# Kernel optimization log

Hardware: AMD Instinct MI355X
Metric: run time of the kernel (lower is better)

## Reference

```python
import jax, jax.numpy as jnp
import numpy as np

V, C, DFF, NH, NL, KS, OUT = 256, 192, 768, 2, 6, 3, 192
B, T, W = 64, 512, 4
DH = C // NH
PAD = KS // 2
DN = ('NCH', 'OIH', 'NCH')


def _rel_to_abs(x):
    # [b,h,l,2l-1] -> [b,h,l,l]  (VITS _relative_position_to_absolute_position)
    b, h, l, _ = x.shape
    x = jnp.pad(x, ((0, 0), (0, 0), (0, 0), (0, 1)))
    x = x.reshape(b, h, l * 2 * l)
    x = jnp.pad(x, ((0, 0), (0, 0), (0, l - 1)))
    x = x.reshape(b, h, l + 1, 2 * l - 1)
    return x[:, :, :l, l - 1:]


def _abs_to_rel(x):
    # [b,h,l,l] -> [b,h,l,2l-1]  (VITS _absolute_position_to_relative_position)
    b, h, l, _ = x.shape
    x = jnp.pad(x, ((0, 0), (0, 0), (0, 0), (0, l - 1)))
    x = x.reshape(b, h, l * (2 * l - 1))
    x = jnp.pad(x, ((0, 0), (0, 0), (l, 0)))
    x = x.reshape(b, h, l, 2 * l)
    return x[:, :, :, 1:]


def _get_rel_emb(emb, length):
    # emb: [2W+1, DH] -> [2*length-1, DH]
    pad_len = max(length - (W + 1), 0)
    start = max(W + 1 - length, 0)
    padded = jnp.pad(emb, ((pad_len, pad_len), (0, 0)))
    return padded[start:start + 2 * length - 1]


def _ln(x, g, b):
    mu = jnp.mean(x, -1, keepdims=True)
    var = jnp.mean(jnp.square(x - mu), -1, keepdims=True)
    return (x - mu) * jax.lax.rsqrt(var + 1e-5) * g + b


def setup_inputs():
    key = jax.random.key(0)
    ks = jax.random.split(key, 12)
    n = lambda k, s, std: jax.random.normal(k, s, jnp.float32) * std
    return dict(
        tokens=jax.random.randint(ks[0], (B, T), 0, V),
        x_lengths=jnp.full((B,), T, dtype=jnp.int32),
        emb_w=n(ks[1], (V, C), C ** -0.5),
        wqkv=n(ks[2], (NL, 3, C, C), 0.02),
        bqkv=jnp.zeros((NL, 3, C), jnp.float32),
        wo=n(ks[3], (NL, C, C), 0.02),
        bo=jnp.zeros((NL, C), jnp.float32),
        rel_k=n(ks[4], (NL, 2 * W + 1, DH), DH ** -0.5),
        rel_v=n(ks[5], (NL, 2 * W + 1, DH), DH ** -0.5),
        ln1_g=jnp.ones((NL, C), jnp.float32),
        ln1_b=jnp.zeros((NL, C), jnp.float32),
        ln2_g=jnp.ones((NL, C), jnp.float32),
        ln2_b=jnp.zeros((NL, C), jnp.float32),
        ffn_w1=n(ks[6], (NL, DFF, C, KS), 0.02),
        ffn_b1=jnp.zeros((NL, DFF), jnp.float32),
        ffn_w2=n(ks[7], (NL, C, DFF, KS), 0.02),
        ffn_b2=jnp.zeros((NL, C), jnp.float32),
        proj_w=n(ks[8], (2 * OUT, C), 0.02),
        proj_b=jnp.zeros((2 * OUT,), jnp.float32),
    )


def reference(tokens, x_lengths, emb_w, wqkv, bqkv, wo, bo, rel_k, rel_v,
              ln1_g, ln1_b, ln2_g, ln2_b, ffn_w1, ffn_b1, ffn_w2, ffn_b2,
              proj_w, proj_b):
    x = emb_w[tokens] * (C ** 0.5)                       # [B,T,C]
    mask = (jnp.arange(T)[None, :] < x_lengths[:, None]).astype(x.dtype)  # [B,T]
    bias = jnp.where((mask[:, None, :, None] * mask[:, None, None, :]) > 0.0, 0.0, -1e4)
    x = x * mask[..., None]
    inv_sqrt_d = DH ** -0.5
    for l in range(NL):
        q = jnp.einsum('btc,oc->bto', x, wqkv[l, 0]) + bqkv[l, 0]
        k = jnp.einsum('btc,oc->bto', x, wqkv[l, 1]) + bqkv[l, 1]
        v = jnp.einsum('btc,oc->bto', x, wqkv[l, 2]) + bqkv[l, 2]
        q = q.reshape(B, T, NH, DH).transpose(0, 2, 1, 3)  # [B,H,T,D]
        k = k.reshape(B, T, NH, DH).transpose(0, 2, 1, 3)
        v = v.reshape(B, T, NH, DH).transpose(0, 2, 1, 3)
        scores = jnp.einsum('bhtd,bhsd->bhts', q, k) * inv_sqrt_d
        rk = _get_rel_emb(rel_k[l], T)                     # [2T-1, D]
        rel_logits = jnp.einsum('bhtd,md->bhtm', q * inv_sqrt_d, rk)
        scores = scores + _rel_to_abs(rel_logits)
        p = jax.nn.softmax(scores + bias, axis=-1)
        o = jnp.einsum('bhts,bhsd->bhtd', p, v)
        o = o + jnp.einsum('bhtm,md->bhtd', _abs_to_rel(p), _get_rel_emb(rel_v[l], T))
        o = o.transpose(0, 2, 1, 3).reshape(B, T, C)
        y = jnp.einsum('btc,oc->bto', o, wo[l]) + bo[l]
        x = _ln(x + y, ln1_g[l], ln1_b[l])
        h = jax.lax.conv_general_dilated((x * mask[..., None]).transpose(0, 2, 1),
                                         ffn_w1[l], (1,), [(PAD, PAD)],
                                         dimension_numbers=DN) + ffn_b1[l][None, :, None]
        h = jax.nn.relu(h) * mask[:, None, :]
        h = jax.lax.conv_general_dilated(h, ffn_w2[l], (1,), [(PAD, PAD)],
                                         dimension_numbers=DN) + ffn_b2[l][None, :, None]
        y = h.transpose(0, 2, 1) * mask[..., None]
        x = _ln(x + y, ln2_g[l], ln2_b[l])
    x = x * mask[..., None]
    stats = (jnp.einsum('btc,oc->bto', x, proj_w) + proj_b) * mask[..., None]
    m, logs = jnp.split(stats, 2, axis=-1)
    x_mask = mask[:, None, :]
    return x.transpose(0, 2, 1), m.transpose(0, 2, 1), logs.transpose(0, 2, 1), x_mask
```

## Files before the change

kernel.cpp:

```cpp
#include <hip/hip_runtime.h>
#include <hip/hip_bf16.h>

typedef __hip_bfloat16 bf16;
typedef __attribute__((ext_vector_type(8))) short short8;
typedef __attribute__((ext_vector_type(4))) float f32x4;

#define NB 64
#define NT 512
#define NC 192
#define NHEAD 2
#define NDH 96
#define NLAYER 6
#define NDFF 768
#define NW 4

constexpr int MROWS = NB * NT;
constexpr size_t MC = (size_t)MROWS * NC;
constexpr size_t MCB = MC * 4;
constexpr float QSC = 0.10206207261596575f * 1.4426950408889634f;

__device__ __forceinline__ float us2f(unsigned short x) { return __uint_as_float((unsigned)x << 16); }
__device__ __forceinline__ unsigned short f2b(float f) {
    bf16 h = __float2bfloat16(f);
    return *reinterpret_cast<unsigned short*>(&h);
}

__global__ __launch_bounds__(256) void cvt_plain(const float* __restrict__ s, bf16* __restrict__ d, int n) {
    int i = blockIdx.x * 256 + threadIdx.x;
    if (i < n) d[i] = __float2bfloat16(s[i]);
}
__global__ __launch_bounds__(256) void cvt_conv(const float* __restrict__ s, bf16* __restrict__ d,
                                                int L, int N, int C) {
    int i = blockIdx.x * 256 + threadIdx.x;
    if (i >= L * N * C * 3) return;
    int dk = i % 3;
    int rest = i / 3;
    int c = rest % C;
    int rest2 = rest / C;
    int n = rest2 % N;
    int l = rest2 / N;
    d[(((size_t)l * 3 + dk) * N + n) * C + c] = __float2bfloat16(s[i]);
}

__global__ __launch_bounds__(256) void embed_kernel(const int* __restrict__ tok,
                                                    const int* __restrict__ lens,
                                                    const float* __restrict__ emb,
                                                    float* __restrict__ x,
                                                    bf16* __restrict__ xb) {
    int idx = blockIdx.x * 256 + threadIdx.x;
    if (idx >= (int)MC) return;
    int c = idx % NC;
    int m = idx / NC;
    int t = m % NT, b = m / NT;
    float v = emb[tok[m] * NC + c] * 13.856406460551018f;
    if (t >= lens[b]) v = 0.f;
    x[idx] = v;
    xb[idx] = __float2bfloat16(v);
}

enum GMode { GM_QKV = 0, GM_CONV1 = 2, GM_PROJ = 4 };

template <int MODE, int NTOT, int KC, int TAPS>
__global__ __launch_bounds__(256) void gemm_mfma(const bf16* __restrict__ A,
                                                 const bf16* __restrict__ W,
                                                 const float* __restrict__ bias,
                                                 const int* __restrict__ lens,
                                                 float* __restrict__ of,
                                                 bf16* __restrict__ ob1,
                                                 bf16* __restrict__ ob2,
                                                 bf16* __restrict__ ob3) {
    constexpr int RA = (TAPS == 3) ? 130 : 128;
    constexpr int RB = TAPS * 64;
    __shared__ unsigned short As[RA * 40];
    __shared__ unsigned short Bs[RB * 40];
    const int tid = threadIdx.x;
    const int w = tid >> 6, lane = tid & 63;
    const int g = lane >> 4, li = lane & 15;
    const int n0 = blockIdx.x * 64;
    const int m0 = blockIdx.y * 128;
    const int b = m0 >> 9, t0 = m0 & 511;
    const int len = lens[b];
    const unsigned short* Au = (const unsigned short*)A;
    const unsigned short* Wu = (const unsigned short*)W;

    f32x4 acc[2][4];
#pragma unroll
    for (int a = 0; a < 2; a++)
#pragma unroll
        for (int s = 0; s < 4; s++) acc[a][s] = (f32x4){0.f, 0.f, 0.f, 0.f};

#pragma unroll 1
    for (int k0 = 0; k0 < KC; k0 += 32) {
        __syncthreads();
        for (int c = tid; c < RA * 2; c += 256) {
            int i = c >> 1, hf = (c & 1) * 16;
            int t = t0 + i - (TAPS == 3 ? 1 : 0);
            bool valid = (t >= 0) && (t < NT);
            if constexpr (MODE == GM_CONV1) valid = valid && (t < len);
            short8 v0{}, v1{};
            if (valid) {
                const unsigned short* src = Au + ((size_t)(b * NT + t) * KC + k0 + hf);
                v0 = *(const short8*)src;
                v1 = *(const short8*)(src + 8);
            }
            *(short8*)&As[i * 40 + hf] = v0;
            *(short8*)&As[i * 40 + hf + 8] = v1;
        }
        for (int c = tid; c < RB * 4; c += 256) {
            int rb = c >> 2, qq = (c & 3) * 8;
            int dk = rb >> 6, nl = rb & 63;
            *(short8*)&Bs[rb * 40 + qq] =
                *(const short8*)(Wu + ((size_t)(dk * NTOT + n0 + nl) * KC + k0 + qq));
        }
        __syncthreads();
#pragma unroll
        for (int dk = 0; dk < TAPS; dk++) {
            short8 af0 = *(const short8*)&As[(w * 32 + li + dk) * 40 + g * 8];
            short8 af1 = *(const short8*)&As[(w * 32 + 16 + li + dk) * 40 + g * 8];
#pragma unroll
            for (int sub = 0; sub < 4; sub++) {
                short8 bfr = *(const short8*)&Bs[(dk * 64 + sub * 16 + li) * 40 + g * 8];
                acc[0][sub] = __builtin_amdgcn_mfma_f32_16x16x32_bf16(af0, bfr, acc[0][sub], 0, 0, 0);
                acc[1][sub] = __builtin_amdgcn_mfma_f32_16x16x32_bf16(af1, bfr, acc[1][sub], 0, 0, 0);
            }
        }
    }

#pragma unroll
    for (int sub = 0; sub < 4; sub++) {
        int n = n0 + sub * 16 + li;
        float bv = bias[n];
#pragma unroll
        for (int a = 0; a < 2; a++) {
#pragma unroll
            for (int rr = 0; rr < 4; rr++) {
                int t = t0 + w * 32 + a * 16 + g * 4 + rr;
                size_t m = (size_t)(b * NT + t);
                float vv = acc[a][sub][rr] + bv;
                if constexpr (MODE == GM_QKV) {
                    int iw = n / NC;
                    int cc = n - iw * NC;
                    int hh = cc >= NDH ? 1 : 0;
                    int d = cc - hh * NDH;
                    int bh = b * NHEAD + hh;
                    if (iw == 0) ob1[((size_t)bh * NT + t) * NDH + d] = __float2bfloat16(vv * QSC);
                    else if (iw == 1) ob2[((size_t)bh * NT + t) * NDH + d] = __float2bfloat16(vv);
                    else ob3[((size_t)bh * NDH + d) * NT + t] = __float2bfloat16(vv);
                } else if constexpr (MODE == GM_CONV1) {
                    vv = vv > 0.f ? vv : 0.f;
                    if (t >= len) vv = 0.f;
                    ob1[m * NDFF + n] = __float2bfloat16(vv);
                } else {
                    if (t >= len) vv = 0.f;
                    int half = n >= 192 ? 1 : 0;
                    int cc = n - half * 192;
                    of[(size_t)(half + 1) * MC + ((size_t)b * NC + cc) * NT + t] = vv;
                }
            }
        }
    }
}

template <int KC, int TAPS, bool MASKY, int BM>
__global__ __launch_bounds__(512) void gemm_ln(const bf16* __restrict__ A,
                                               const bf16* __restrict__ W,
                                               const float* __restrict__ bias,
                                               const int* __restrict__ lens,
                                               const float* __restrict__ lng,
                                               const float* __restrict__ lnb,
                                               float* __restrict__ x,
                                               bf16* __restrict__ xb) {
    constexpr int RA = BM + ((TAPS == 3) ? 2 : 0);
    constexpr int RB = TAPS * 192;
    constexpr int NSTEP = KC / 32;
    constexpr int NBI = (RB * 4 + 511) / 512;
    constexpr int AR = BM / 32;
    __shared__ unsigned short As[RA * 40];
    __shared__ unsigned short Bs[RB * 40];
    __shared__ float rsm[BM][4];
    __shared__ float rsq[BM][4];
    const int tid = threadIdx.x;
    const int lane = tid & 63;
    const int g = lane >> 4, li = lane & 15;
    const int w = tid >> 6;
    const int wr = w & 1, wc = w >> 1;
    const int m0 = blockIdx.x * BM;
    const int b = m0 >> 9, t0 = m0 & 511;
    const int len = lens[b];
    const unsigned short* Au = (const unsigned short*)A;
    const unsigned short* Wu = (const unsigned short*)W;

    const int ai = tid >> 1, ahf = (tid & 1) * 16;
    const int at = t0 + ai - (TAPS == 3 ? 1 : 0);
    const bool aon = (tid < RA * 2);
    const bool avalid = aon && (at >= 0) && (at < NT);

    short8 ra0{}, ra1{};
    short8 rbv[NBI];
#pragma unroll
    for (int j = 0; j < NBI; j++) rbv[j] = short8{};

    f32x4 acc[AR][3];
#pragma unroll
    for (int ar = 0; ar < AR; ar++)
#pragma unroll
        for (int sub = 0; sub < 3; sub++) acc[ar][sub] = (f32x4){0.f, 0.f, 0.f, 0.f};

    if (avalid) {
        const unsigned short* src = Au + ((size_t)(b * NT + at) * KC + 0 + ahf);
        ra0 = *(const short8*)src;
        ra1 = *(const short8*)(src + 8);
    }
#pragma unroll
    for (int j = 0; j < NBI; j++) {
        int cb = tid + j * 512;
        if (cb < RB * 4) {
            int rbr = cb >> 2, qq = (cb & 3) * 8;
            rbv[j] = *(const short8*)(Wu + ((size_t)rbr * KC + 0 + qq));
        }
    }
    if (aon) {
        short8 z{};
        *(short8*)&As[ai * 40 + ahf] = avalid ? ra0 : z;
        *(short8*)&As[ai * 40 + ahf + 8] = avalid ? ra1 : z;
    }
#pragma unroll
    for (int j = 0; j < NBI; j++) {
        int cb = tid + j * 512;
        if (cb < RB * 4) {
            int rbr = cb >> 2, qq = (cb & 3) * 8;
            *(short8*)&Bs[rbr * 40 + qq] = rbv[j];
        }
    }

#pragma unroll 1
    for (int s = 0; s < NSTEP; s++) {
        __syncthreads();
        if (s + 1 < NSTEP) {
            int k0 = (s + 1) * 32;
            if (avalid) {
                const unsigned short* src = Au + ((size_t)(b * NT + at) * KC + k0 + ahf);
                ra0 = *(const short8*)src;
                ra1 = *(const short8*)(src + 8);
            }
#pragma unroll
            for (int j = 0; j < NBI; j++) {
                int cb = tid + j * 512;
                if (cb < RB * 4) {
                    int rbr = cb >> 2, qq = (cb & 3) * 8;
                    rbv[j] = *(const short8*)(Wu + ((size_t)rbr * KC + k0 + qq));
                }
            }
        }
#pragma unroll
        for (int dk = 0; dk < TAPS; dk++) {
            short8 af[AR];
#pragma unroll
            for (int ar = 0; ar < AR; ar++)
                af[ar] = *(const short8*)&As[(wr * (BM / 2) + ar * 16 + li + dk) * 40 + g * 8];
#pragma unroll
            for (int sub = 0; sub < 3; sub++) {
                short8 bfr = *(const short8*)&Bs[(dk * 192 + wc * 48 + sub * 16 + li) * 40 + g * 8];
#pragma unroll
                for (int ar = 0; ar < AR; ar++)
                    acc[ar][sub] = __builtin_amdgcn_mfma_f32_16x16x32_bf16(af[ar], bfr, acc[ar][sub], 0, 0, 0);
            }
        }
        __syncthreads();
        if (s + 1 < NSTEP) {
            if (aon) {
                short8 z{};
                *(short8*)&As[ai * 40 + ahf] = avalid ? ra0 : z;
                *(short8*)&As[ai * 40 + ahf + 8] = avalid ? ra1 : z;
            }
#pragma unroll
            for (int j = 0; j < NBI; j++) {
                int cb = tid + j * 512;
                if (cb < RB * 4) {
                    int rbr = cb >> 2, qq = (cb & 3) * 8;
                    *(short8*)&Bs[rbr * 40 + qq] = rbv[j];
                }
            }
        }
    }

    float biasv[3], gv[3], bbv[3];
#pragma unroll
    for (int sub = 0; sub < 3; sub++) {
        int n = wc * 48 + sub * 16 + li;
        biasv[sub] = bias[n];
        gv[sub] = lng[n];
        bbv[sub] = lnb[n];
    }
    float psm[AR][4], psq[AR][4];
#pragma unroll
    for (int ar = 0; ar < AR; ar++) {
#pragma unroll
        for (int rr = 0; rr < 4; rr++) {
            int r = wr * (BM / 2) + ar * 16 + 4 * g + rr;
            int t = t0 + r;
            size_t m = (size_t)(b * NT + t);
            float sm = 0.f, sq = 0.f;
#pragma unroll
            for (int sub = 0; sub < 3; sub++) {
                int n = wc * 48 + sub * 16 + li;
                float y = acc[ar][sub][rr] + biasv[sub];
                if (MASKY && t >= len) y = 0.f;
                float rres = y + x[m * NC + n];
                acc[ar][sub][rr] = rres;
                sm += rres;
                sq += rres * rres;
            }
            psm[ar][rr] = sm;
            psq[ar][rr] = sq;
        }
    }
#pragma unroll
    for (int off = 1; off < 16; off <<= 1) {
#pragma unroll
        for (int ar = 0; ar < AR; ar++)
#pragma unroll
            for (int rr = 0; rr < 4; rr++) {
                psm[ar][rr] += __shfl_xor(psm[ar][rr], off);
                psq[ar][rr] += __shfl_xor(psq[ar][rr], off);
            }
    }
    if (li == 0) {
#pragma unroll
        for (int ar = 0; ar < AR; ar++)
#pragma unroll
            for (int rr = 0; rr < 4; rr++) {
                int r = wr * (BM / 2) + ar * 16 + 4 * g + rr;
                rsm[r][wc] = psm[ar][rr];
                rsq[r][wc] = psq[ar][rr];
            }
    }
    __syncthreads();
#pragma unroll
    for (int ar = 0; ar < AR; ar++) {
#pragma unroll
        for (int rr = 0; rr < 4; rr++) {
            int r = wr * (BM / 2) + ar * 16 + 4 * g + rr;
            int t = t0 + r;
            size_t m = (size_t)(b * NT + t);
            float sm = rsm[r][0] + rsm[r][1] + rsm[r][2] + rsm[r][3];
            float sq = rsq[r][0] + rsq[r][1] + rsq[r][2] + rsq[r][3];
            float mu = sm * (1.f / NC);
            float var = fmaxf(sq * (1.f / NC) - mu * mu, 0.f);
            float rs = rsqrtf(var + 1e-5f);
#pragma unroll
            for (int sub = 0; sub < 3; sub++) {
                int n = wc * 48 + sub * 16 + li;
                float o = (acc[ar][sub][rr] - mu) * rs * gv[sub] + bbv[sub];
                x[m * NC + n] = o;
                xb[m * NC + n] = __float2bfloat16(o);
            }
        }
    }
}

__global__ __launch_bounds__(256, 4) void attn_mfma(const bf16* __restrict__ q,
                                                    const bf16* __restrict__ k,
                                                    const bf16* __restrict__ v,
                                                    const float* __restrict__ relk,
                                                    const float* __restrict__ relv,
                                                    const int* __restrict__ lens,
                                                    bf16* __restrict__ o) {
    __shared__ __align__(16) char pool[40448];
    unsigned short* Kt = (unsigned short*)pool;
    unsigned short* Vt = (unsigned short*)(pool + 13312);
    unsigned short* Pt = (unsigned short*)(pool + 27136);
    unsigned short* Pb = (unsigned short*)(pool + 36352);
    unsigned short* Qt = (unsigned short*)pool;
    unsigned short* Rk = (unsigned short*)(pool + 13312);

    const int bh = blockIdx.x, qt = blockIdx.y;
    const int b = bh >> 1, h = bh & 1;
    const int q0 = qt * 64;
    const int tid = threadIdx.x;
    const int w = tid >> 6, lane = tid & 63;
    const int g = lane >> 4, li = lane & 15;
    const int len = lens[b];
    const bool anymask = (len < NT);

    const unsigned short* qg = (const unsigned short*)q + (size_t)bh * NT * NDH;
    const unsigned short* kg = (const unsigned short*)k + (size_t)bh * NT * NDH;
    const unsigned short* vg = (const unsigned short*)v + (size_t)bh * NDH * NT;

    for (int c = tid; c < 64 * 12; c += 256) {
        int r = c / 12, seg = (c % 12) * 8;
        *(short8*)&Qt[r * 104 + seg] = *(const short8*)(qg + (size_t)(q0 + r) * NDH + seg);
    }
    for (int c = tid; c < 16 * 96; c += 256) {
        int dd = c / 96, d = c - (c / 96) * 96;
        Rk[dd * 104 + d] = (dd < 9) ? f2b(relk[dd * 96 + d]) : (unsigned short)0;
    }
    for (int c = tid; c < 4 * 16 * 32; c += 256) Pb[c] = 0;
    __syncthreads();

    f32x4 racc = (f32x4){0.f, 0.f, 0.f, 0.f};
    short8 qf[3];
#pragma unroll
    for (int kk = 0; kk < 3; kk++) {
        qf[kk] = *(const short8*)&Qt[(w * 16 + li) * 104 + kk * 32 + g * 8];
        short8 bfr = *(const short8*)&Rk[li * 104 + kk * 32 + g * 8];
        racc = __builtin_amdgcn_mfma_f32_16x16x32_bf16(qf[kk], bfr, racc, 0, 0, 0);
    }
    short8 rvf[6];
#pragma unroll
    for (int ds = 0; ds < 6; ds++) {
#pragma unroll
        for (int i = 0; i < 8; i++) {
            int j = g * 8 + i;
            int d = ds * 16 + li;
            unsigned short u = (j < 9) ? f2b(relv[j * 96 + d]) : (unsigned short)0;
            rvf[ds][i] = (short)u;
        }
    }
    __syncthreads();

    float m_run[4], l_run[4];
    f32x4 Oa[6];
#pragma unroll
    for (int rr = 0; rr < 4; rr++) { m_run[rr] = -1e30f; l_run[rr] = 0.f; }
#pragma unroll
    for (int ds = 0; ds < 6; ds++) Oa[ds] = (f32x4){0.f, 0.f, 0.f, 0.f};

    const int wrow0 = q0 + w * 16;

    for (int s0 = 0; s0 < NT; s0 += 64) {
        for (int c = tid; c < 64 * 12; c += 256) {
            int ss = c / 12, seg = (c % 12) * 8;
            *(short8*)&Kt[ss * 104 + seg] = *(const short8*)(kg + (size_t)(s0 + ss) * NDH + seg);
        }
        for (int c = tid; c < 96 * 8; c += 256) {
            int d = c >> 3, seg = (c & 7) * 8;
            *(short8*)&Vt[d * 72 + seg] = *(const short8*)(vg + (size_t)d * NT + s0 + seg);
        }
        __syncthreads();

        const bool band = (s0 <= wrow0 + 15 + NW) && (s0 + 63 >= wrow0 - NW);

        f32x4 acc[4];
#pragma unroll
        for (int sub = 0; sub < 4; sub++) acc[sub] = (f32x4){0.f, 0.f, 0.f, 0.f};
        __builtin_amdgcn_s_setprio(1);
#pragma unroll
        for (int kk = 0; kk < 3; kk++) {
#pragma unroll
            for (int sub = 0; sub < 4; sub++) {
                short8 bfr = *(const short8*)&Kt[(sub * 16 + li) * 104 + kk * 32 + g * 8];
                acc[sub] = __builtin_amdgcn_mfma_f32_16x16x32_bf16(qf[kk], bfr, acc[sub], 0, 0, 0);
            }
        }
        __builtin_amdgcn_s_setprio(0);

        if (band) {
#pragma unroll
            for (int sub = 0; sub < 4; sub++) {
#pragma unroll
                for (int rr = 0; rr < 4; rr++) {
                    int scol = s0 + sub * 16 + li;
                    int qrow = wrow0 + 4 * g + rr;
                    int dd = scol - qrow;
                    float rv = __shfl(racc[rr], g * 16 + dd + NW);
                    if (dd >= -NW && dd <= NW) acc[sub][rr] += rv;
                }
            }
        }
        float rmax[4];
#pragma unroll
        for (int rr = 0; rr < 4; rr++) rmax[rr] = -1e30f;
#pragma unroll
        for (int sub = 0; sub < 4; sub++) {
#pragma unroll
            for (int rr = 0; rr < 4; rr++) {
                if (anymask) {
                    int scol = s0 + sub * 16 + li;
                    int qrow = wrow0 + 4 * g + rr;
                    if (scol >= len || qrow >= len) acc[sub][rr] -= 14427.0f;
                }
                rmax[rr] = fmaxf(rmax[rr], acc[sub][rr]);
            }
        }
#pragma unroll
        for (int off = 1; off < 16; off <<= 1)
#pragma unroll
            for (int rr = 0; rr < 4; rr++) rmax[rr] = fmaxf(rmax[rr], __shfl_xor(rmax[rr], off));

        float growth = -3.0e38f;
#pragma unroll
        for (int rr = 0; rr < 4; rr++) growth = fmaxf(growth, rmax[rr] - m_run[rr]);
        if (__any(growth > 11.54f)) {
#pragma unroll
            for (int rr = 0; rr < 4; rr++) {
                float mn = fmaxf(m_run[rr], rmax[rr]);
                float scf = exp2f(m_run[rr] - mn);
                m_run[rr] = mn;
                l_run[rr] *= scf;
#pragma unroll
                for (int ds = 0; ds < 6; ds++) Oa[ds][rr] *= scf;
            }
        }
        float rsum[4] = {0.f, 0.f, 0.f, 0.f};
#pragma unroll
        for (int sub = 0; sub < 4; sub++)
#pragma unroll
            for (int rr = 0; rr < 4; rr++) {
                float p = exp2f(acc[sub][rr] - m_run[rr]);
                acc[sub][rr] = p;
                rsum[rr] += p;
            }
#pragma unroll
        for (int off = 1; off < 16; off <<= 1)
#pragma unroll
            for (int rr = 0; rr < 4; rr++) rsum[rr] += __shfl_xor(rsum[rr], off);
#pragma unroll
        for (int rr = 0; rr < 4; rr++) l_run[rr] += rsum[rr];

#pragma unroll
        for (int sub = 0; sub < 4; sub++)
#pragma unroll
            for (int rr = 0; rr < 4; rr++)
                Pt[w * 1152 + (4 * g + rr) * 72 + sub * 16 + li] = f2b(acc[sub][rr]);

        __builtin_amdgcn_s_setprio(1);
#pragma unroll
        for (int kk = 0; kk < 2; kk++) {
            short8 pa = *(const short8*)&Pt[w * 1152 + li * 72 + kk * 32 + g * 8];
#pragma unroll
            for (int ds = 0; ds < 6; ds++) {
                short8 bv = *(const short8*)&Vt[(ds * 16 + li) * 72 + kk * 32 + g * 8];
                Oa[ds] = __builtin_amdgcn_mfma_f32_16x16x32_bf16(pa, bv, Oa[ds], 0, 0, 0);
            }
        }
        __builtin_amdgcn_s_setprio(0);

        if (band) {
            for (int j = g; j < 9; j += 4) {
                int u = wrow0 + li + j - NW - s0;
                unsigned short pv_ = (u >= 0 && u < 64) ? Pt[w * 1152 + li * 72 + u] : (unsigned short)0;
                Pb[w * 512 + li * 32 + j] = pv_;
            }
            short8 pband = *(const short8*)&Pb[w * 512 + li * 32 + g * 8];
#pragma unroll
            for (int ds = 0; ds < 6; ds++)
                Oa[ds] = __builtin_amdgcn_mfma_f32_16x16x32_bf16(pband, rvf[ds], Oa[ds], 0, 0, 0);
        }
        __syncthreads();
    }

    float invl[4];
#pragma unroll
    for (int rr = 0; rr < 4; rr++) invl[rr] = 1.f / l_run[rr];
#pragma unroll
    for (int ds = 0; ds < 6; ds++)
#pragma unroll
        for (int rr = 0; rr < 4; rr++) {
            int qrow = wrow0 + 4 * g + rr;
            o[((size_t)(b * NT + qrow)) * NC + h * 96 + ds * 16 + li] =
                __float2bfloat16(Oa[ds][rr] * invl[rr]);
        }
}

__global__ __launch_bounds__(256) void xpose_kernel(const float* __restrict__ x,
                                                    const int* __restrict__ lens,
                                                    float* __restrict__ out) {
    int idx = blockIdx.x * 256 + threadIdx.x;
    if (idx >= (int)MC) return;
    int t = idx % NT;
    int bc = idx / NT;
    int c = bc % NC;
    int b = bc / NC;
    float v = (t < lens[b]) ? x[((size_t)b * NT + t) * NC + c] : 0.f;
    out[idx] = v;
}

__global__ __launch_bounds__(256) void mask_kernel(const int* __restrict__ lens, float* __restrict__ out) {
    int idx = blockIdx.x * 256 + threadIdx.x;
    if (idx >= NB * NT) return;
    int t = idx % NT;
    int b = idx / NT;
    out[idx] = (t < lens[b]) ? 1.f : 0.f;
}

extern "C" void kernel_launch(void* const* d_in, const int* in_sizes, int n_in,
                              void* d_out, int out_size, void* d_ws, size_t ws_size,
                              hipStream_t stream) {
    (void)in_sizes; (void)n_in; (void)out_size; (void)ws_size;
    const int* tok = (const int*)d_in[0];
    const int* lens = (const int*)d_in[1];
    const float* emb = (const float*)d_in[2];
    const float* wqkv = (const float*)d_in[3];
    const float* bqkv = (const float*)d_in[4];
    const float* wo = (const float*)d_in[5];
    const float* bo = (const float*)d_in[6];
    const float* relk = (const float*)d_in[7];
    const float* relv = (const float*)d_in[8];
    const float* ln1g = (const float*)d_in[9];
    const float* ln1b = (const float*)d_in[10];
    const float* ln2g = (const float*)d_in[11];
    const float* ln2b = (const float*)d_in[12];
    const float* fw1 = (const float*)d_in[13];
    const float* fb1 = (const float*)d_in[14];
    const float* fw2 = (const float*)d_in[15];
    const float* fb2 = (const float*)d_in[16];
    const float* pw = (const float*)d_in[17];
    const float* pb = (const float*)d_in[18];
    float* out = (float*)d_out;

    char* wsb = (char*)d_ws;
    float* xB = (float*)wsb;
    bf16* xb = (bf16*)(wsb + 2 * MCB);
    bf16* qb = (bf16*)(wsb + 2 * MCB + MCB / 2);
    bf16* kb = qb + MC;
    bf16* vb = kb + MC;
    bf16* ob = vb + MC;
    bf16* hB = qb;
    bf16* pwqkv = ob + MC;
    bf16* pwo = pwqkv + (size_t)NLAYER * 3 * NC * NC;
    bf16* pw1 = pwo + (size_t)NLAYER * NC * NC;
    bf16* pw2 = pw1 + (size_t)NLAYER * 3 * NDFF * NC;
    bf16* pproj = pw2 + (size_t)NLAYER * 3 * NC * NDFF;

    {
        int n1 = NLAYER * 3 * NC * NC;
        cvt_plain<<<(n1 + 255) / 256, 256, 0, stream>>>(wqkv, pwqkv, n1);
        int n2 = NLAYER * NC * NC;
        cvt_plain<<<(n2 + 255) / 256, 256, 0, stream>>>(wo, pwo, n2);
        int n3 = 2 * 192 * NC;
        cvt_plain<<<(n3 + 255) / 256, 256, 0, stream>>>(pw, pproj, n3);
        int n4 = NLAYER * NDFF * NC * 3;
        cvt_conv<<<(n4 + 255) / 256, 256, 0, stream>>>(fw1, pw1, NLAYER, NDFF, NC);
        int n5 = NLAYER * NC * NDFF * 3;
        cvt_conv<<<(n5 + 255) / 256, 256, 0, stream>>>(fw2, pw2, NLAYER, NC, NDFF);
    }

    embed_kernel<<<(int)((MC + 255) / 256), 256, 0, stream>>>(tok, lens, emb, xB, xb);

    for (int l = 0; l < NLAYER; l++) {
        gemm_mfma<GM_QKV, 576, 192, 1><<<dim3(9, 256), 256, 0, stream>>>(
            xb, pwqkv + (size_t)l * 3 * NC * NC, bqkv + (size_t)l * 3 * NC, lens,
            nullptr, qb, kb, vb);
        attn_mfma<<<dim3(NB * NHEAD, 8), 256, 0, stream>>>(
            qb, kb, vb, relk + (size_t)l * (2 * NW + 1) * NDH,
            relv + (size_t)l * (2 * NW + 1) * NDH, lens, ob);
        gemm_ln<192, 1, false, 64><<<512, 512, 0, stream>>>(
            ob, pwo + (size_t)l * NC * NC, bo + (size_t)l * NC, lens,
            ln1g + (size_t)l * NC, ln1b + (size_t)l * NC, xB, xb);
        gemm_mfma<GM_CONV1, 768, 192, 3><<<dim3(12, 256), 256, 0, stream>>>(
            xb, pw1 + (size_t)l * 3 * NDFF * NC, fb1 + (size_t)l * NDFF, lens,
            nullptr, hB, nullptr, nullptr);
        gemm_ln<768, 3, true, 64><<<512, 512, 0, stream>>>(
            hB, pw2 + (size_t)l * 3 * NC * NDFF, fb2 + (size_t)l * NC, lens,
            ln2g + (size_t)l * NC, ln2b + (size_t)l * NC, xB, xb);
    }

    gemm_mfma<GM_PROJ, 384, 192, 1><<<dim3(6, 256), 256, 0, stream>>>(
        xb, pproj, pb, lens, out, nullptr, nullptr, nullptr);
    xpose_kernel<<<(int)((MC + 255) / 256), 256, 0, stream>>>(xB, lens, out);
    mask_kernel<<<(NB * NT + 255) / 256, 256, 0, stream>>>(lens, out + 3 * MC);
}
```

Baseline: 1.507 ms.

## Pre-swizzle weights into MFMA fragment order and load B directly from global

Weight conversion kernels now write bf16 weights in a per-lane MFMA fragment layout, so each lane can fetch its B operand with a single 16-byte global load. Both GEMM kernels drop the shared-memory B tile and its staging loops, and gemm_ln double-buffers B fragments in registers across K steps. gemm_ln also gets a min-blocks hint of 4 in its launch bounds. This removes LDS traffic and LDS capacity for weights, at the cost of more registers and repeated global or L2 reads of the weights by every wave.

After: 1.448 ms. 1.04x faster.

```diff
diff --git a/kernel.cpp b/kernel.cpp
--- a/kernel.cpp
+++ b/kernel.cpp
@@ -25,21 +25,43 @@
     return *reinterpret_cast<unsigned short*>(&h);
 }
 
-__global__ __launch_bounds__(256) void cvt_plain(const float* __restrict__ s, bf16* __restrict__ d, int n) {
+__global__ __launch_bounds__(256) void cvt_frag_plain(const float* __restrict__ s, bf16* __restrict__ d,
+                                                      int L, int N, int K) {
     int i = blockIdx.x * 256 + threadIdx.x;
-    if (i < n) d[i] = __float2bfloat16(s[i]);
-}
-__global__ __launch_bounds__(256) void cvt_conv(const float* __restrict__ s, bf16* __restrict__ d,
-                                                int L, int N, int C) {
+    int total = L * (N / 16) * (K / 32) * 64;
+    if (i >= total) return;
+    int lane = i & 63;
+    int tile = i >> 6;
+    int nbk = K / 32;
+    int kb = tile % nbk;
+    int rest = tile / nbk;
+    int nb = rest % (N / 16);
+    int l = rest / (N / 16);
+    int li = lane & 15, g = lane >> 4;
+    const float* src = s + ((size_t)l * N + nb * 16 + li) * K + kb * 32 + g * 8;
+    bf16* dst = d + (size_t)i * 8;
+#pragma unroll
+    for (int u = 0; u < 8; u++) dst[u] = __float2bfloat16(src[u]);
+}
+__global__ __launch_bounds__(256) void cvt_frag_conv(const float* __restrict__ s, bf16* __restrict__ d,
+                                                     int L, int N, int C) {
     int i = blockIdx.x * 256 + threadIdx.x;
-    if (i >= L * N * C * 3) return;
-    int dk = i % 3;
-    int rest = i / 3;
-    int c = rest % C;
-    int rest2 = rest / C;
-    int n = rest2 % N;
-    int l = rest2 / N;
-    d[(((size_t)l * 3 + dk) * N + n) * C + c] = __float2bfloat16(s[i]);
+    int total = L * 3 * (N / 16) * (C / 32) * 64;
+    if (i >= total) return;
+    int lane = i & 63;
+    int tile = i >> 6;
+    int nbk = C / 32;
+    int kb = tile % nbk;
+    int rest = tile / nbk;
+    int nb = rest % (N / 16);
+    int rest2 = rest / (N / 16);
+    int dk = rest2 % 3;
+    int l = rest2 / 3;
+    int li = lane & 15, g = lane >> 4;
+    const float* src = s + (((size_t)l * N + nb * 16 + li) * C + kb * 32 + g * 8) * 3 + dk;
+    bf16* dst = d + (size_t)i * 8;
+#pragma unroll
+    for (int u = 0; u < 8; u++) dst[u] = __float2bfloat16(src[u * 3]);
 }
 
 __global__ __launch_bounds__(256) void embed_kernel(const int* __restrict__ tok,
@@ -70,9 +92,9 @@
                                                  bf16* __restrict__ ob2,
                                                  bf16* __restrict__ ob3) {
     constexpr int RA = (TAPS == 3) ? 130 : 128;
-    constexpr int RB = TAPS * 64;
+    constexpr int NBN = NTOT / 16;
+    constexpr int NBK = KC / 32;
     __shared__ unsigned short As[RA * 40];
-    __shared__ unsigned short Bs[RB * 40];
     const int tid = threadIdx.x;
     const int w = tid >> 6, lane = tid & 63;
     const int g = lane >> 4, li = lane & 15;
@@ -80,6 +102,7 @@
     const int m0 = blockIdx.y * 128;
     const int b = m0 >> 9, t0 = m0 & 511;
     const int len = lens[b];
+    const int nbBase = n0 >> 4;
     const unsigned short* Au = (const unsigned short*)A;
     const unsigned short* Wu = (const unsigned short*)W;
 
@@ -91,6 +114,7 @@
 
 #pragma unroll 1
     for (int k0 = 0; k0 < KC; k0 += 32) {
+        const int kb = k0 >> 5;
         __syncthreads();
         for (int c = tid; c < RA * 2; c += 256) {
             int i = c >> 1, hf = (c & 1) * 16;
@@ -106,12 +130,6 @@
             *(short8*)&As[i * 40 + hf] = v0;
             *(short8*)&As[i * 40 + hf + 8] = v1;
         }
-        for (int c = tid; c < RB * 4; c += 256) {
-            int rb = c >> 2, qq = (c & 3) * 8;
-            int dk = rb >> 6, nl = rb & 63;
-            *(short8*)&Bs[rb * 40 + qq] =
-                *(const short8*)(Wu + ((size_t)(dk * NTOT + n0 + nl) * KC + k0 + qq));
-        }
         __syncthreads();
 #pragma unroll
         for (int dk = 0; dk < TAPS; dk++) {
@@ -119,7 +137,8 @@
             short8 af1 = *(const short8*)&As[(w * 32 + 16 + li + dk) * 40 + g * 8];
 #pragma unroll
             for (int sub = 0; sub < 4; sub++) {
-                short8 bfr = *(const short8*)&Bs[(dk * 64 + sub * 16 + li) * 40 + g * 8];
+                short8 bfr = *(const short8*)(Wu +
+                    ((((size_t)(dk * NBN + nbBase + sub)) * NBK + kb) << 9) + (lane << 3));
                 acc[0][sub] = __builtin_amdgcn_mfma_f32_16x16x32_bf16(af0, bfr, acc[0][sub], 0, 0, 0);
                 acc[1][sub] = __builtin_amdgcn_mfma_f32_16x16x32_bf16(af1, bfr, acc[1][sub], 0, 0, 0);
             }
@@ -162,21 +181,20 @@
 }
 
 template <int KC, int TAPS, bool MASKY, int BM>
-__global__ __launch_bounds__(512) void gemm_ln(const bf16* __restrict__ A,
-                                               const bf16* __restrict__ W,
-                                               const float* __restrict__ bias,
-                                               const int* __restrict__ lens,
-                                               const float* __restrict__ lng,
-                                               const float* __restrict__ lnb,
-                                               float* __restrict__ x,
-                                               bf16* __restrict__ xb) {
+__global__ __launch_bounds__(512, 4) void gemm_ln(const bf16* __restrict__ A,
+                                                  const bf16* __restrict__ W,
+                                                  const float* __restrict__ bias,
+                                                  const int* __restrict__ lens,
+                                                  const float* __restrict__ lng,
+                                                  const float* __restrict__ lnb,
+                                                  float* __restrict__ x,
+                                                  bf16* __restrict__ xb) {
     constexpr int RA = BM + ((TAPS == 3) ? 2 : 0);
-    constexpr int RB = TAPS * 192;
     constexpr int NSTEP = KC / 32;
-    constexpr int NBI = (RB * 4 + 511) / 512;
+    constexpr int NBN = 12;
+    constexpr int NBK = KC / 32;
     constexpr int AR = BM / 32;
     __shared__ unsigned short As[RA * 40];
-    __shared__ unsigned short Bs[RB * 40];
     __shared__ float rsm[BM][4];
     __shared__ float rsq[BM][4];
     const int tid = threadIdx.x;
@@ -196,9 +214,7 @@
     const bool avalid = aon && (at >= 0) && (at < NT);
 
     short8 ra0{}, ra1{};
-    short8 rbv[NBI];
-#pragma unroll
-    for (int j = 0; j < NBI; j++) rbv[j] = short8{};
+    short8 bcur[TAPS][3], bnxt[TAPS][3];
 
     f32x4 acc[AR][3];
 #pragma unroll
@@ -212,25 +228,15 @@
         ra1 = *(const short8*)(src + 8);
     }
 #pragma unroll
-    for (int j = 0; j < NBI; j++) {
-        int cb = tid + j * 512;
-        if (cb < RB * 4) {
-            int rbr = cb >> 2, qq = (cb & 3) * 8;
-            rbv[j] = *(const short8*)(Wu + ((size_t)rbr * KC + 0 + qq));
-        }
-    }
+    for (int dk = 0; dk < TAPS; dk++)
+#pragma unroll
+        for (int sub = 0; sub < 3; sub++)
+            bcur[dk][sub] = *(const short8*)(Wu +
+                ((((size_t)(dk * NBN + wc * 3 + sub)) * NBK) << 9) + (lane << 3));
     if (aon) {
         short8 z{};
         *(short8*)&As[ai * 40 + ahf] = avalid ? ra0 : z;
         *(short8*)&As[ai * 40 + ahf + 8] = avalid ? ra1 : z;
-    }
-#pragma unroll
-    for (int j = 0; j < NBI; j++) {
-        int cb = tid + j * 512;
-        if (cb < RB * 4) {
-            int rbr = cb >> 2, qq = (cb & 3) * 8;
-            *(short8*)&Bs[rbr * 40 + qq] = rbv[j];
-        }
     }
 
 #pragma unroll 1
@@ -244,13 +250,11 @@
                 ra1 = *(const short8*)(src + 8);
             }
 #pragma unroll
-            for (int j = 0; j < NBI; j++) {
-                int cb = tid + j * 512;
-                if (cb < RB * 4) {
-                    int rbr = cb >> 2, qq = (cb & 3) * 8;
-                    rbv[j] = *(const short8*)(Wu + ((size_t)rbr * KC + k0 + qq));
-                }
-            }
+            for (int dk = 0; dk < TAPS; dk++)
+#pragma unroll
+                for (int sub = 0; sub < 3; sub++)
+                    bnxt[dk][sub] = *(const short8*)(Wu +
+                        ((((size_t)(dk * NBN + wc * 3 + sub)) * NBK + (s + 1)) << 9) + (lane << 3));
         }
 #pragma unroll
         for (int dk = 0; dk < TAPS; dk++) {
@@ -260,10 +264,9 @@
                 af[ar] = *(const short8*)&As[(wr * (BM / 2) + ar * 16 + li + dk) * 40 + g * 8];
 #pragma unroll
             for (int sub = 0; sub < 3; sub++) {
-                short8 bfr = *(const short8*)&Bs[(dk * 192 + wc * 48 + sub * 16 + li) * 40 + g * 8];
 #pragma unroll
                 for (int ar = 0; ar < AR; ar++)
-                    acc[ar][sub] = __builtin_amdgcn_mfma_f32_16x16x32_bf16(af[ar], bfr, acc[ar][sub], 0, 0, 0);
+                    acc[ar][sub] = __builtin_amdgcn_mfma_f32_16x16x32_bf16(af[ar], bcur[dk][sub], acc[ar][sub], 0, 0, 0);
             }
         }
         __syncthreads();
@@ -274,13 +277,9 @@
                 *(short8*)&As[ai * 40 + ahf + 8] = avalid ? ra1 : z;
             }
 #pragma unroll
-            for (int j = 0; j < NBI; j++) {
-                int cb = tid + j * 512;
-                if (cb < RB * 4) {
-                    int rbr = cb >> 2, qq = (cb & 3) * 8;
-                    *(short8*)&Bs[rbr * 40 + qq] = rbv[j];
-                }
-            }
+            for (int dk = 0; dk < TAPS; dk++)
+#pragma unroll
+                for (int sub = 0; sub < 3; sub++) bcur[dk][sub] = bnxt[dk][sub];
         }
     }
 
@@ -624,16 +623,16 @@
     bf16* pproj = pw2 + (size_t)NLAYER * 3 * NC * NDFF;
 
     {
-        int n1 = NLAYER * 3 * NC * NC;
-        cvt_plain<<<(n1 + 255) / 256, 256, 0, stream>>>(wqkv, pwqkv, n1);
-        int n2 = NLAYER * NC * NC;
-        cvt_plain<<<(n2 + 255) / 256, 256, 0, stream>>>(wo, pwo, n2);
-        int n3 = 2 * 192 * NC;
-        cvt_plain<<<(n3 + 255) / 256, 256, 0, stream>>>(pw, pproj, n3);
-        int n4 = NLAYER * NDFF * NC * 3;
-        cvt_conv<<<(n4 + 255) / 256, 256, 0, stream>>>(fw1, pw1, NLAYER, NDFF, NC);
-        int n5 = NLAYER * NC * NDFF * 3;
-        cvt_conv<<<(n5 + 255) / 256, 256, 0, stream>>>(fw2, pw2, NLAYER, NC, NDFF);
+        int n1 = NLAYER * 36 * 6 * 64;
+        cvt_frag_plain<<<(n1 + 255) / 256, 256, 0, stream>>>(wqkv, pwqkv, NLAYER, 576, 192);
+        int n2 = NLAYER * 12 * 6 * 64;
+        cvt_frag_plain<<<(n2 + 255) / 256, 256, 0, stream>>>(wo, pwo, NLAYER, 192, 192);
+        int n3 = 1 * 24 * 6 * 64;
+        cvt_frag_plain<<<(n3 + 255) / 256, 256, 0, stream>>>(pw, pproj, 1, 384, 192);
+        int n4 = NLAYER * 3 * 48 * 6 * 64;
+        cvt_frag_conv<<<(n4 + 255) / 256, 256, 0, stream>>>(fw1, pw1, NLAYER, 768, 192);
+        int n5 = NLAYER * 3 * 12 * 24 * 64;
+        cvt_frag_conv<<<(n5 + 255) / 256, 256, 0, stream>>>(fw2, pw2, NLAYER, 192, 768);
     }
 
     embed_kernel<<<(int)((MC + 255) / 256), 256, 0, stream>>>(tok, lens, emb, xB, xb);
```
